# Optimization experiments

Measured on AMD Instinct MI355X. Metric: run time of the kernel, lower is better.

The kernel has to match this reference:

```python
import jax, jax.numpy as jnp
import numpy as np

B, A, F, C = 32, 64, 128, 128


def _mlp(h, W0, b0, W1, b1):
    # LinearLayer stack: Linear(2F->C) + ReLU, Linear(C->C) + ReLU
    h = jax.nn.relu(h @ W0 + b0)
    h = jax.nn.relu(h @ W1 + b1)
    return h


def setup_inputs() -> dict:
    key = jax.random.key(0)
    k0, k1, k2 = jax.random.split(key, 3)
    x = jax.random.normal(k0, (B, A, F), dtype=jnp.float32)
    W0 = jax.random.normal(k1, (2 * F, C), dtype=jnp.float32) * (1.0 / np.sqrt(2 * F))
    b0 = jnp.zeros((C,), dtype=jnp.float32)
    W1 = jax.random.normal(k2, (C, C), dtype=jnp.float32) * (1.0 / np.sqrt(C))
    b1 = jnp.zeros((C,), dtype=jnp.float32)
    return {"x": x, "W0": W0, "b0": b0, "W1": W1, "b1": b1}


def reference(x, W0, b0, W1, b1):
    nb, na, nf = x.shape
    # atom_tile[b,i,j]   = x[b,i]  (first atom of the pair)
    # atom_repeat[b,i,j] = x[b,j]  (second atom of the pair)
    xi = jnp.broadcast_to(x[:, :, None, :], (nb, na, na, nf))
    xj = jnp.broadcast_to(x[:, None, :, :], (nb, na, na, nf))
    # pair_x0 = cat(atom_tile, atom_repeat) = [x_i, x_j]
    p0 = jnp.concatenate([xi, xj], axis=-1).reshape(nb * na * na, 2 * nf)
    # pair_x1 = cat(atom_repeat, atom_tile) = [x_j, x_i]
    p1 = jnp.concatenate([xj, xi], axis=-1).reshape(nb * na * na, 2 * nf)
    h0 = _mlp(p0, W0, b0, W1, b1).reshape(nb, na * na, -1)
    h1 = _mlp(p1, W0, b0, W1, b1).reshape(nb, na * na, -1)
    return h0 + h1
```

## Files before the change

kernel.cpp:

```cpp
#include <hip/hip_runtime.h>
#include <hip/hip_bf16.h>

typedef float    f32x4 __attribute__((ext_vector_type(4)));
typedef _Float16 f16x4 __attribute__((ext_vector_type(4)));
typedef _Float16 f16x8 __attribute__((ext_vector_type(8)));
typedef unsigned int   u32x4 __attribute__((ext_vector_type(4)));

#define NB 32
#define NA 64
#define NF 128
#define NC 128

__global__ __launch_bounds__(256) void prep_kernel(
    const float* __restrict__ x, const float* __restrict__ W0,
    const float* __restrict__ b0, const float* __restrict__ W1,
    _Float16* __restrict__ u, _Float16* __restrict__ v,
    _Float16* __restrict__ w1f)
{
    int blk = blockIdx.x, tid = threadIdx.x;
    if (blk < 256) {
        __shared__ __align__(16) _Float16 w0h[32 * 64 * 8];
        int b = blk >> 3, g = (blk >> 1) & 3, half = blk & 1;

        int lane = tid & 63, wave = tid >> 6;
        int llo = lane & 15, lhi = lane >> 4;

        const float* xrow = x + ((size_t)b * NA + g * 16 + llo) * NF;
        f16x8 xf[4];
        #pragma unroll
        for (int kk = 0; kk < 4; ++kk) {
            f32x4 a0 = *(const f32x4*)(xrow + kk * 32 + lhi * 8);
            f32x4 a1 = *(const f32x4*)(xrow + kk * 32 + lhi * 8 + 4);
            #pragma unroll
            for (int e = 0; e < 4; ++e) {
                xf[kk][e]     = (_Float16)a0[e];
                xf[kk][e + 4] = (_Float16)a1[e];
            }
        }

        #pragma unroll
        for (int p = 0; p < 8; ++p) {
            int sl   = p * 256 + tid;
            int frag = sl >> 6;
            int ln   = sl & 63;
            int kk   = frag >> 3, nfc = frag & 7;
            int k0   = half * 128 + kk * 32 + (ln >> 4) * 8;
            int c    = nfc * 16 + (ln & 15);
            f16x8 o;
            #pragma unroll
            for (int e = 0; e < 8; ++e)
                o[e] = (_Float16)W0[(size_t)(k0 + e) * NC + c];
            *(f16x8*)(w0h + (size_t)sl * 8) = o;
        }
        __syncthreads();

        f32x4 acc[2];
        f32x4 z = {0.f, 0.f, 0.f, 0.f};
        acc[0] = z; acc[1] = z;
        #pragma unroll
        for (int kk = 0; kk < 4; ++kk) {
            #pragma unroll
            for (int t = 0; t < 2; ++t) {
                int nfc = wave * 2 + t;
                f16x8 aw = *(const f16x8*)(w0h +
                    (size_t)((kk * 8 + nfc) * 64 + lane) * 8);
                acc[t] = __builtin_amdgcn_mfma_f32_16x16x32_f16(
                    aw, xf[kk], acc[t], 0, 0, 0);
            }
        }

        _Float16* dst = half ? v : u;
        size_t arow = ((size_t)b * NA + g * 16 + llo) * NC;
        #pragma unroll
        for (int t = 0; t < 2; ++t) {
            int nfc = wave * 2 + t;
            int c0  = nfc * 16 + lhi * 4;
            f16x4 o;
            if (half) {
                f32x4 bb = *(const f32x4*)(b0 + c0);
                #pragma unroll
                for (int e = 0; e < 4; ++e)
                    o[e] = (_Float16)(acc[t][e] + bb[e]);
            } else {
                #pragma unroll
                for (int e = 0; e < 4; ++e)
                    o[e] = (_Float16)acc[t][e];
            }
            *(f16x4*)(dst + arow + c0) = o;
        }
    } else {
        int fl   = (blk - 256) * 256 + tid;
        int lane = fl & 63;
        int frag = fl >> 6;
        int kk = frag >> 3, nf = frag & 7;
        int k0 = kk * 32 + (lane >> 4) * 8;
        int n  = nf * 16 + (lane & 15);
        f16x8 o;
        #pragma unroll
        for (int e = 0; e < 8; ++e)
            o[e] = (_Float16)W1[(size_t)(k0 + e) * NC + n];
        *(f16x8*)(w1f + (size_t)fl * 8) = o;
    }
}

__global__ __launch_bounds__(256, 3) void pair_mlp_kernel(
    const float* __restrict__ b1g, const _Float16* __restrict__ u,
    const _Float16* __restrict__ v, const _Float16* __restrict__ w1f,
    float* __restrict__ out)
{
    __shared__ __align__(16) _Float16 u_s[16 * 128];
    __shared__ __align__(16) _Float16 v_s[16 * 128];
    __shared__ __align__(16) _Float16 w_s[32 * 64 * 8];

    int blk = blockIdx.x;
    int b = blk / 36;
    int t = blk % 36;
    int I = 0;
    while (t >= 8 - I) { t -= 8 - I; ++I; }
    int J = I + t;

    int tid = threadIdx.x;

    {
        int row = tid >> 4;
        int c   = tid & 15;
        int ga  = b * NA + ((row < 8) ? (I * 8 + row) : (J * 8 + (row & 7)));
        int sc  = row * 16 + (c ^ (row & 7));
        ((u32x4*)u_s)[sc] = ((const u32x4*)(u + (size_t)ga * NC))[c];
        ((u32x4*)v_s)[sc] = ((const u32x4*)(v + (size_t)ga * NC))[c];
    }
    #pragma unroll
    for (int p = 0; p < 8; ++p)
        ((u32x4*)w_s)[p * 256 + tid] = ((const u32x4*)w1f)[p * 256 + tid];
    __syncthreads();

    int wave = tid >> 6;
    int lane = tid & 63;
    int llo  = lane & 15;
    int lhi  = lane >> 4;
    int r    = wave * 16 + llo;
    int il   = r >> 3;
    int jl   = r & 7;

    f32x4 acc0[8], acc1[8];
    f32x4 z = {0.f, 0.f, 0.f, 0.f};
    #pragma unroll
    for (int nf = 0; nf < 8; ++nf) { acc0[nf] = z; acc1[nf] = z; }

    const f16x8* us = (const f16x8*)u_s;
    const f16x8* vs = (const f16x8*)v_s;
    const f16x8* wf = (const f16x8*)w_s;

    #pragma unroll
    for (int kk = 0; kk < 4; ++kk) {
        int kc  = kk * 4 + lhi;
        int scI = il * 16 + (kc ^ il);
        int scJ = (8 + jl) * 16 + (kc ^ jl);

        f16x8 uIv = us[scI];
        f16x8 vIv = vs[scI];
        f16x8 uJv = us[scJ];
        f16x8 vJv = vs[scJ];

        f16x8 s0 = uIv + vJv;
        f16x8 s1 = uJv + vIv;
        f16x8 h0, h1;
        #pragma unroll
        for (int e = 0; e < 8; ++e) {
            h0[e] = s0[e] < (_Float16)0 ? (_Float16)0 : s0[e];
            h1[e] = s1[e] < (_Float16)0 ? (_Float16)0 : s1[e];
        }

        #pragma unroll
        for (int nf = 0; nf < 8; ++nf) {
            f16x8 w = wf[(kk * 8 + nf) * 64 + lane];
            acc0[nf] = __builtin_amdgcn_mfma_f32_16x16x32_f16(w, h0, acc0[nf], 0, 0, 0);
            acc1[nf] = __builtin_amdgcn_mfma_f32_16x16x32_f16(w, h1, acc1[nf], 0, 0, 0);
        }
    }

    int Ig = I * 8 + il;
    int Jg = J * 8 + jl;
    float* p1 = out + ((size_t)b * 4096 + Ig * 64 + Jg) * 128 + lhi * 4;
    float* p2 = out + ((size_t)b * 4096 + Jg * 64 + Ig) * 128 + lhi * 4;
    bool mirror = (I != J);
    #pragma unroll
    for (int nf = 0; nf < 8; ++nf) {
        f32x4 bias = *(const f32x4*)(b1g + nf * 16 + lhi * 4);
        f32x4 val;
        #pragma unroll
        for (int e = 0; e < 4; ++e)
            val[e] = fmaxf(acc0[nf][e] + bias[e], 0.f) +
                     fmaxf(acc1[nf][e] + bias[e], 0.f);
        *(f32x4*)(p1 + nf * 16) = val;
        if (mirror)
            *(f32x4*)(p2 + nf * 16) = val;
    }
}

extern "C" void kernel_launch(void* const* d_in, const int* in_sizes, int n_in,
                              void* d_out, int out_size, void* d_ws, size_t ws_size,
                              hipStream_t stream)
{
    (void)in_sizes; (void)n_in; (void)out_size; (void)ws_size;
    const float* x  = (const float*)d_in[0];
    const float* W0 = (const float*)d_in[1];
    const float* b0 = (const float*)d_in[2];
    const float* W1 = (const float*)d_in[3];
    const float* b1 = (const float*)d_in[4];
    float* out = (float*)d_out;

    _Float16* u   = (_Float16*)d_ws;
    _Float16* v   = u + (size_t)NB * NA * NC;
    _Float16* w1f = v + (size_t)NB * NA * NC;

    prep_kernel<<<264, 256, 0, stream>>>(x, W0, b0, W1, u, v, w1f);
    pair_mlp_kernel<<<32 * 36, 256, 0, stream>>>(b1, u, v, w1f, out);
}
```

Before: 29.90 us.

## Keep W1 fragments in registers and drop symmetric-pair tiling in pair MLP

```diff
diff --git a/kernel.cpp b/kernel.cpp
--- a/kernel.cpp
+++ b/kernel.cpp
@@ -103,98 +103,93 @@
     }
 }
 
-__global__ __launch_bounds__(256, 3) void pair_mlp_kernel(
+__global__ __launch_bounds__(512, 2) void pair_mlp_kernel(
     const float* __restrict__ b1g, const _Float16* __restrict__ u,
     const _Float16* __restrict__ v, const _Float16* __restrict__ w1f,
     float* __restrict__ out)
 {
-    __shared__ __align__(16) _Float16 u_s[16 * 128];
-    __shared__ __align__(16) _Float16 v_s[16 * 128];
-    __shared__ __align__(16) _Float16 w_s[32 * 64 * 8];
+    __shared__ __align__(16) _Float16 u_s[64 * 128];
+    __shared__ __align__(16) _Float16 v_s[64 * 128];
 
     int blk = blockIdx.x;
-    int b = blk / 36;
-    int t = blk % 36;
-    int I = 0;
-    while (t >= 8 - I) { t -= 8 - I; ++I; }
-    int J = I + t;
-
-    int tid = threadIdx.x;
-
-    {
-        int row = tid >> 4;
-        int c   = tid & 15;
-        int ga  = b * NA + ((row < 8) ? (I * 8 + row) : (J * 8 + (row & 7)));
+    int b  = blk >> 3;
+    int Iq = blk & 7;
+    int tid  = threadIdx.x;
+    int wave = tid >> 6, lane = tid & 63;
+    int llo  = lane & 15, lhi = lane >> 4;
+
+    f16x8 wreg[4][8];
+    #pragma unroll
+    for (int kk = 0; kk < 4; ++kk)
+        #pragma unroll
+        for (int nf = 0; nf < 8; ++nf)
+            wreg[kk][nf] = ((const f16x8*)w1f)[(kk * 8 + nf) * 64 + lane];
+
+    #pragma unroll
+    for (int p = 0; p < 2; ++p) {
+        int idx = p * 512 + tid;
+        int row = idx >> 4;
+        int c   = idx & 15;
         int sc  = row * 16 + (c ^ (row & 7));
-        ((u32x4*)u_s)[sc] = ((const u32x4*)(u + (size_t)ga * NC))[c];
-        ((u32x4*)v_s)[sc] = ((const u32x4*)(v + (size_t)ga * NC))[c];
+        ((u32x4*)u_s)[sc] = ((const u32x4*)(u + ((size_t)b * NA + row) * NC))[c];
+        ((u32x4*)v_s)[sc] = ((const u32x4*)(v + ((size_t)b * NA + row) * NC))[c];
     }
-    #pragma unroll
-    for (int p = 0; p < 8; ++p)
-        ((u32x4*)w_s)[p * 256 + tid] = ((const u32x4*)w1f)[p * 256 + tid];
     __syncthreads();
 
-    int wave = tid >> 6;
-    int lane = tid & 63;
-    int llo  = lane & 15;
-    int lhi  = lane >> 4;
-    int r    = wave * 16 + llo;
-    int il   = r >> 3;
-    int jl   = r & 7;
-
-    f32x4 acc0[8], acc1[8];
-    f32x4 z = {0.f, 0.f, 0.f, 0.f};
-    #pragma unroll
-    for (int nf = 0; nf < 8; ++nf) { acc0[nf] = z; acc1[nf] = z; }
-
+    int ai = Iq * 8 + wave;
     const f16x8* us = (const f16x8*)u_s;
     const f16x8* vs = (const f16x8*)v_s;
-    const f16x8* wf = (const f16x8*)w_s;
-
-    #pragma unroll
-    for (int kk = 0; kk < 4; ++kk) {
-        int kc  = kk * 4 + lhi;
-        int scI = il * 16 + (kc ^ il);
-        int scJ = (8 + jl) * 16 + (kc ^ jl);
-
-        f16x8 uIv = us[scI];
-        f16x8 vIv = vs[scI];
-        f16x8 uJv = us[scJ];
-        f16x8 vJv = vs[scJ];
-
-        f16x8 s0 = uIv + vJv;
-        f16x8 s1 = uJv + vIv;
-        f16x8 h0, h1;
-        #pragma unroll
-        for (int e = 0; e < 8; ++e) {
-            h0[e] = s0[e] < (_Float16)0 ? (_Float16)0 : s0[e];
-            h1[e] = s1[e] < (_Float16)0 ? (_Float16)0 : s1[e];
-        }
-
+    float* orow = out + ((size_t)b * 4096 + (size_t)ai * 64) * 128;
+
+    f32x4 z = {0.f, 0.f, 0.f, 0.f};
+
+    for (int q = 0; q < 4; ++q) {
+        int aj = q * 16 + llo;
+
+        f32x4 acc0[8], acc1[8];
+        #pragma unroll
+        for (int nf = 0; nf < 8; ++nf) { acc0[nf] = z; acc1[nf] = z; }
+
+        #pragma unroll
+        for (int kk = 0; kk < 4; ++kk) {
+            int kc  = kk * 4 + lhi;
+            int sci = ai * 16 + (kc ^ (ai & 7));
+            int scj = aj * 16 + (kc ^ (aj & 7));
+
+            f16x8 ui = us[sci];
+            f16x8 vi = vs[sci];
+            f16x8 uj = us[scj];
+            f16x8 vj = vs[scj];
+
+            f16x8 s0 = ui + vj;
+            f16x8 s1 = uj + vi;
+            f16x8 h0, h1;
+            #pragma unroll
+            for (int e = 0; e < 8; ++e) {
+                h0[e] = s0[e] < (_Float16)0 ? (_Float16)0 : s0[e];
+                h1[e] = s1[e] < (_Float16)0 ? (_Float16)0 : s1[e];
+            }
+
+            #pragma unroll
+            for (int nf = 0; nf < 8; ++nf) {
+                acc0[nf] = __builtin_amdgcn_mfma_f32_16x16x32_f16(
+                    wreg[kk][nf], h0, acc0[nf], 0, 0, 0);
+                acc1[nf] = __builtin_amdgcn_mfma_f32_16x16x32_f16(
+                    wreg[kk][nf], h1, acc1[nf], 0, 0, 0);
+            }
+        }
+
+        float* p1 = orow + (size_t)(q * 16 + llo) * 128 + lhi * 4;
         #pragma unroll
         for (int nf = 0; nf < 8; ++nf) {
-            f16x8 w = wf[(kk * 8 + nf) * 64 + lane];
-            acc0[nf] = __builtin_amdgcn_mfma_f32_16x16x32_f16(w, h0, acc0[nf], 0, 0, 0);
-            acc1[nf] = __builtin_amdgcn_mfma_f32_16x16x32_f16(w, h1, acc1[nf], 0, 0, 0);
-        }
-    }
-
-    int Ig = I * 8 + il;
-    int Jg = J * 8 + jl;
-    float* p1 = out + ((size_t)b * 4096 + Ig * 64 + Jg) * 128 + lhi * 4;
-    float* p2 = out + ((size_t)b * 4096 + Jg * 64 + Ig) * 128 + lhi * 4;
-    bool mirror = (I != J);
-    #pragma unroll
-    for (int nf = 0; nf < 8; ++nf) {
-        f32x4 bias = *(const f32x4*)(b1g + nf * 16 + lhi * 4);
-        f32x4 val;
-        #pragma unroll
-        for (int e = 0; e < 4; ++e)
-            val[e] = fmaxf(acc0[nf][e] + bias[e], 0.f) +
-                     fmaxf(acc1[nf][e] + bias[e], 0.f);
-        *(f32x4*)(p1 + nf * 16) = val;
-        if (mirror)
-            *(f32x4*)(p2 + nf * 16) = val;
+            f32x4 bias = *(const f32x4*)(b1g + nf * 16 + lhi * 4);
+            f32x4 val;
+            #pragma unroll
+            for (int e = 0; e < 4; ++e)
+                val[e] = fmaxf(acc0[nf][e] + bias[e], 0.f) +
+                         fmaxf(acc1[nf][e] + bias[e], 0.f);
+            *(f32x4*)(p1 + nf * 16) = val;
+        }
     }
 }
 
@@ -215,5 +210,5 @@
     _Float16* w1f = v + (size_t)NB * NA * NC;
 
     prep_kernel<<<264, 256, 0, stream>>>(x, W0, b0, W1, u, v, w1f);
-    pair_mlp_kernel<<<32 * 36, 256, 0, stream>>>(b1, u, v, w1f, out);
+    pair_mlp_kernel<<<NB * 8, 512, 0, stream>>>(b1, u, v, w1f, out);
 }
```

Result: slower. 36.50 us (+22.1%).

## Fuse prep and pair-MLP kernels into one persistent kernel with grid barrier

Applied to the files above, without the earlier changes.

```diff
diff --git a/kernel.cpp b/kernel.cpp
--- a/kernel.cpp
+++ b/kernel.cpp
@@ -10,20 +10,28 @@
 #define NA 64
 #define NF 128
 #define NC 128
-
-__global__ __launch_bounds__(256) void prep_kernel(
+#define NBLK 576
+
+__global__ __launch_bounds__(256, 3) void fused_kernel(
     const float* __restrict__ x, const float* __restrict__ W0,
     const float* __restrict__ b0, const float* __restrict__ W1,
-    _Float16* __restrict__ u, _Float16* __restrict__ v,
-    _Float16* __restrict__ w1f)
+    const float* __restrict__ b1g, _Float16* __restrict__ u,
+    _Float16* __restrict__ v, _Float16* __restrict__ w1f,
+    unsigned int* __restrict__ cnt, float* __restrict__ out)
 {
+    __shared__ __align__(16) unsigned char smem[40960];
+    _Float16* w0h = (_Float16*)smem;
+    _Float16* u_s = (_Float16*)smem;
+    _Float16* v_s = (_Float16*)(smem + 4096);
+    _Float16* w_s = (_Float16*)(smem + 8192);
+
     int blk = blockIdx.x, tid = threadIdx.x;
+    int lane = tid & 63, wave = tid >> 6;
+    int llo = lane & 15, lhi = lane >> 4;
+    f32x4 z = {0.f, 0.f, 0.f, 0.f};
+
     if (blk < 256) {
-        __shared__ __align__(16) _Float16 w0h[32 * 64 * 8];
         int b = blk >> 3, g = (blk >> 1) & 3, half = blk & 1;
-
-        int lane = tid & 63, wave = tid >> 6;
-        int llo = lane & 15, lhi = lane >> 4;
 
         const float* xrow = x + ((size_t)b * NA + g * 16 + llo) * NF;
         f16x8 xf[4];
@@ -55,7 +63,6 @@
         __syncthreads();
 
         f32x4 acc[2];
-        f32x4 z = {0.f, 0.f, 0.f, 0.f};
         acc[0] = z; acc[1] = z;
         #pragma unroll
         for (int kk = 0; kk < 4; ++kk) {
@@ -88,113 +95,116 @@
             }
             *(f16x4*)(dst + arow + c0) = o;
         }
-    } else {
+    } else if (blk < 264) {
         int fl   = (blk - 256) * 256 + tid;
-        int lane = fl & 63;
+        int ln   = fl & 63;
         int frag = fl >> 6;
         int kk = frag >> 3, nf = frag & 7;
-        int k0 = kk * 32 + (lane >> 4) * 8;
-        int n  = nf * 16 + (lane & 15);
+        int k0 = kk * 32 + (ln >> 4) * 8;
+        int n  = nf * 16 + (ln & 15);
         f16x8 o;
         #pragma unroll
         for (int e = 0; e < 8; ++e)
             o[e] = (_Float16)W1[(size_t)(k0 + e) * NC + n];
         *(f16x8*)(w1f + (size_t)fl * 8) = o;
     }
-}
-
-__global__ __launch_bounds__(256, 3) void pair_mlp_kernel(
-    const float* __restrict__ b1g, const _Float16* __restrict__ u,
-    const _Float16* __restrict__ v, const _Float16* __restrict__ w1f,
-    float* __restrict__ out)
-{
-    __shared__ __align__(16) _Float16 u_s[16 * 128];
-    __shared__ __align__(16) _Float16 v_s[16 * 128];
-    __shared__ __align__(16) _Float16 w_s[32 * 64 * 8];
-
-    int blk = blockIdx.x;
-    int b = blk / 36;
-    int t = blk % 36;
-    int I = 0;
-    while (t >= 8 - I) { t -= 8 - I; ++I; }
-    int J = I + t;
-
-    int tid = threadIdx.x;
-
-    {
-        int row = tid >> 4;
-        int c   = tid & 15;
-        int ga  = b * NA + ((row < 8) ? (I * 8 + row) : (J * 8 + (row & 7)));
-        int sc  = row * 16 + (c ^ (row & 7));
-        ((u32x4*)u_s)[sc] = ((const u32x4*)(u + (size_t)ga * NC))[c];
-        ((u32x4*)v_s)[sc] = ((const u32x4*)(v + (size_t)ga * NC))[c];
+
+    __syncthreads();
+    if (tid == 0) {
+        __builtin_amdgcn_fence(__ATOMIC_RELEASE, "agent");
+        __hip_atomic_fetch_add(cnt, 1u, __ATOMIC_RELAXED,
+                               __HIP_MEMORY_SCOPE_AGENT);
+        while (__hip_atomic_load(cnt, __ATOMIC_RELAXED,
+                                 __HIP_MEMORY_SCOPE_AGENT) < NBLK)
+            __builtin_amdgcn_s_sleep(1);
+        __builtin_amdgcn_fence(__ATOMIC_ACQUIRE, "agent");
     }
+    __syncthreads();
+
     #pragma unroll
     for (int p = 0; p < 8; ++p)
         ((u32x4*)w_s)[p * 256 + tid] = ((const u32x4*)w1f)[p * 256 + tid];
-    __syncthreads();
-
-    int wave = tid >> 6;
-    int lane = tid & 63;
-    int llo  = lane & 15;
-    int lhi  = lane >> 4;
-    int r    = wave * 16 + llo;
-    int il   = r >> 3;
-    int jl   = r & 7;
-
-    f32x4 acc0[8], acc1[8];
-    f32x4 z = {0.f, 0.f, 0.f, 0.f};
-    #pragma unroll
-    for (int nf = 0; nf < 8; ++nf) { acc0[nf] = z; acc1[nf] = z; }
-
-    const f16x8* us = (const f16x8*)u_s;
-    const f16x8* vs = (const f16x8*)v_s;
-    const f16x8* wf = (const f16x8*)w_s;
-
-    #pragma unroll
-    for (int kk = 0; kk < 4; ++kk) {
-        int kc  = kk * 4 + lhi;
-        int scI = il * 16 + (kc ^ il);
-        int scJ = (8 + jl) * 16 + (kc ^ jl);
-
-        f16x8 uIv = us[scI];
-        f16x8 vIv = vs[scI];
-        f16x8 uJv = us[scJ];
-        f16x8 vJv = vs[scJ];
-
-        f16x8 s0 = uIv + vJv;
-        f16x8 s1 = uJv + vIv;
-        f16x8 h0, h1;
-        #pragma unroll
-        for (int e = 0; e < 8; ++e) {
-            h0[e] = s0[e] < (_Float16)0 ? (_Float16)0 : s0[e];
-            h1[e] = s1[e] < (_Float16)0 ? (_Float16)0 : s1[e];
-        }
-
+
+    #pragma unroll 1
+    for (int s = 0; s < 2; ++s) {
+        int task = blk * 2 + s;
+        int b = task / 36;
+        int t = task % 36;
+        int I = 0;
+        while (t >= 8 - I) { t -= 8 - I; ++I; }
+        int J = I + t;
+
+        if (s) __syncthreads();
+
+        {
+            int row = tid >> 4;
+            int c   = tid & 15;
+            int ga  = b * NA + ((row < 8) ? (I * 8 + row) : (J * 8 + (row & 7)));
+            int sc  = row * 16 + (c ^ (row & 7));
+            ((u32x4*)u_s)[sc] = ((const u32x4*)(u + (size_t)ga * NC))[c];
+            ((u32x4*)v_s)[sc] = ((const u32x4*)(v + (size_t)ga * NC))[c];
+        }
+        __syncthreads();
+
+        int r  = wave * 16 + llo;
+        int il = r >> 3;
+        int jl = r & 7;
+
+        f32x4 acc0[8], acc1[8];
+        #pragma unroll
+        for (int nf = 0; nf < 8; ++nf) { acc0[nf] = z; acc1[nf] = z; }
+
+        const f16x8* us = (const f16x8*)u_s;
+        const f16x8* vs = (const f16x8*)v_s;
+        const f16x8* wf = (const f16x8*)w_s;
+
+        #pragma unroll
+        for (int kk = 0; kk < 4; ++kk) {
+            int kc  = kk * 4 + lhi;
+            int scI = il * 16 + (kc ^ il);
+            int scJ = (8 + jl) * 16 + (kc ^ jl);
+
+            f16x8 uIv = us[scI];
+            f16x8 vIv = vs[scI];
+            f16x8 uJv = us[scJ];
+            f16x8 vJv = vs[scJ];
+
+            f16x8 s0 = uIv + vJv;
+            f16x8 s1 = uJv + vIv;
+            f16x8 h0, h1;
+            #pragma unroll
+            for (int e = 0; e < 8; ++e) {
+                h0[e] = s0[e] < (_Float16)0 ? (_Float16)0 : s0[e];
+                h1[e] = s1[e] < (_Float16)0 ? (_Float16)0 : s1[e];
+            }
+
+            #pragma unroll
+            for (int nf = 0; nf < 8; ++nf) {
+                f16x8 w = wf[(kk * 8 + nf) * 64 + lane];
+                acc0[nf] = __builtin_amdgcn_mfma_f32_16x16x32_f16(
+                    w, h0, acc0[nf], 0, 0, 0);
+                acc1[nf] = __builtin_amdgcn_mfma_f32_16x16x32_f16(
+                    w, h1, acc1[nf], 0, 0, 0);
+            }
+        }
+
+        int Ig = I * 8 + il;
+        int Jg = J * 8 + jl;
+        float* p1 = out + ((size_t)b * 4096 + Ig * 64 + Jg) * 128 + lhi * 4;
+        float* p2 = out + ((size_t)b * 4096 + Jg * 64 + Ig) * 128 + lhi * 4;
+        bool mirror = (I != J);
         #pragma unroll
         for (int nf = 0; nf < 8; ++nf) {
-            f16x8 w = wf[(kk * 8 + nf) * 64 + lane];
-            acc0[nf] = __builtin_amdgcn_mfma_f32_16x16x32_f16(w, h0, acc0[nf], 0, 0, 0);
-            acc1[nf] = __builtin_amdgcn_mfma_f32_16x16x32_f16(w, h1, acc1[nf], 0, 0, 0);
-        }
-    }
-
-    int Ig = I * 8 + il;
-    int Jg = J * 8 + jl;
-    float* p1 = out + ((size_t)b * 4096 + Ig * 64 + Jg) * 128 + lhi * 4;
-    float* p2 = out + ((size_t)b * 4096 + Jg * 64 + Ig) * 128 + lhi * 4;
-    bool mirror = (I != J);
-    #pragma unroll
-    for (int nf = 0; nf < 8; ++nf) {
-        f32x4 bias = *(const f32x4*)(b1g + nf * 16 + lhi * 4);
-        f32x4 val;
-        #pragma unroll
-        for (int e = 0; e < 4; ++e)
-            val[e] = fmaxf(acc0[nf][e] + bias[e], 0.f) +
-                     fmaxf(acc1[nf][e] + bias[e], 0.f);
-        *(f32x4*)(p1 + nf * 16) = val;
-        if (mirror)
-            *(f32x4*)(p2 + nf * 16) = val;
+            f32x4 bias = *(const f32x4*)(b1g + nf * 16 + lhi * 4);
+            f32x4 val;
+            #pragma unroll
+            for (int e = 0; e < 4; ++e)
+                val[e] = fmaxf(acc0[nf][e] + bias[e], 0.f) +
+                         fmaxf(acc1[nf][e] + bias[e], 0.f);
+            *(f32x4*)(p1 + nf * 16) = val;
+            if (mirror)
+                *(f32x4*)(p2 + nf * 16) = val;
+        }
     }
 }
 
@@ -213,7 +223,9 @@
     _Float16* u   = (_Float16*)d_ws;
     _Float16* v   = u + (size_t)NB * NA * NC;
     _Float16* w1f = v + (size_t)NB * NA * NC;
-
-    prep_kernel<<<264, 256, 0, stream>>>(x, W0, b0, W1, u, v, w1f);
-    pair_mlp_kernel<<<32 * 36, 256, 0, stream>>>(b1, u, v, w1f, out);
+    unsigned int* cnt = (unsigned int*)(w1f + 32 * 64 * 8);
+
+    hipMemsetAsync(cnt, 0, sizeof(unsigned int), stream);
+    fused_kernel<<<NBLK, 256, 0, stream>>>(x, W0, b0, W1, b1, u, v, w1f,
+                                           cnt, out);
 }
```

After: 79.76 us. 167% more time.

## Process two pair tiles per block and coalesce W0 staging via swizzled LDS

Applied to the files above, without the earlier changes.

```diff
diff --git a/kernel.cpp b/kernel.cpp
--- a/kernel.cpp
+++ b/kernel.cpp
@@ -18,12 +18,12 @@
     _Float16* __restrict__ w1f)
 {
     int blk = blockIdx.x, tid = threadIdx.x;
+    int lane = tid & 63, wave = tid >> 6;
+    int llo = lane & 15, lhi = lane >> 4;
+
     if (blk < 256) {
-        __shared__ __align__(16) _Float16 w0h[32 * 64 * 8];
+        __shared__ __align__(16) _Float16 w0l[128 * 128];
         int b = blk >> 3, g = (blk >> 1) & 3, half = blk & 1;
-
-        int lane = tid & 63, wave = tid >> 6;
-        int llo = lane & 15, lhi = lane >> 4;
 
         const float* xrow = x + ((size_t)b * NA + g * 16 + llo) * NF;
         f16x8 xf[4];
@@ -38,19 +38,22 @@
             }
         }
 
+        const float* w0src = W0 + (size_t)half * 128 * NC;
         #pragma unroll
         for (int p = 0; p < 8; ++p) {
-            int sl   = p * 256 + tid;
-            int frag = sl >> 6;
-            int ln   = sl & 63;
-            int kk   = frag >> 3, nfc = frag & 7;
-            int k0   = half * 128 + kk * 32 + (ln >> 4) * 8;
-            int c    = nfc * 16 + (ln & 15);
+            int idx = p * 256 + tid;
+            int k   = idx >> 4;
+            int ch  = idx & 15;
+            f32x4 a0 = *(const f32x4*)(w0src + (size_t)k * NC + ch * 8);
+            f32x4 a1 = *(const f32x4*)(w0src + (size_t)k * NC + ch * 8 + 4);
             f16x8 o;
             #pragma unroll
-            for (int e = 0; e < 8; ++e)
-                o[e] = (_Float16)W0[(size_t)(k0 + e) * NC + c];
-            *(f16x8*)(w0h + (size_t)sl * 8) = o;
+            for (int e = 0; e < 4; ++e) {
+                o[e]     = (_Float16)a0[e];
+                o[e + 4] = (_Float16)a1[e];
+            }
+            int sc = (ch ^ ((k >> 3) & 7)) << 3;
+            *(f16x8*)(w0l + k * 128 + sc) = o;
         }
         __syncthreads();
 
@@ -62,8 +65,16 @@
             #pragma unroll
             for (int t = 0; t < 2; ++t) {
                 int nfc = wave * 2 + t;
-                f16x8 aw = *(const f16x8*)(w0h +
-                    (size_t)((kk * 8 + nfc) * 64 + lane) * 8);
+                int c   = nfc * 16 + llo;
+                int chx = (c >> 3);
+                int cl  = c & 7;
+                f16x8 aw;
+                #pragma unroll
+                for (int e = 0; e < 8; ++e) {
+                    int k = kk * 32 + lhi * 8 + e;
+                    int sc = ((chx ^ ((k >> 3) & 7)) << 3) | cl;
+                    aw[e] = w0l[k * 128 + sc];
+                }
                 acc[t] = __builtin_amdgcn_mfma_f32_16x16x32_f16(
                     aw, xf[kk], acc[t], 0, 0, 0);
             }
@@ -90,11 +101,11 @@
         }
     } else {
         int fl   = (blk - 256) * 256 + tid;
-        int lane = fl & 63;
+        int ln   = fl & 63;
         int frag = fl >> 6;
         int kk = frag >> 3, nf = frag & 7;
-        int k0 = kk * 32 + (lane >> 4) * 8;
-        int n  = nf * 16 + (lane & 15);
+        int k0 = kk * 32 + (ln >> 4) * 8;
+        int n  = nf * 16 + (ln & 15);
         f16x8 o;
         #pragma unroll
         for (int e = 0; e < 8; ++e)
@@ -103,7 +114,7 @@
     }
 }
 
-__global__ __launch_bounds__(256, 3) void pair_mlp_kernel(
+__global__ __launch_bounds__(256, 4) void pair_mlp_kernel(
     const float* __restrict__ b1g, const _Float16* __restrict__ u,
     const _Float16* __restrict__ v, const _Float16* __restrict__ w1f,
     float* __restrict__ out)
@@ -112,89 +123,95 @@
     __shared__ __align__(16) _Float16 v_s[16 * 128];
     __shared__ __align__(16) _Float16 w_s[32 * 64 * 8];
 
-    int blk = blockIdx.x;
-    int b = blk / 36;
-    int t = blk % 36;
-    int I = 0;
-    while (t >= 8 - I) { t -= 8 - I; ++I; }
-    int J = I + t;
-
-    int tid = threadIdx.x;
-
-    {
-        int row = tid >> 4;
-        int c   = tid & 15;
-        int ga  = b * NA + ((row < 8) ? (I * 8 + row) : (J * 8 + (row & 7)));
-        int sc  = row * 16 + (c ^ (row & 7));
-        ((u32x4*)u_s)[sc] = ((const u32x4*)(u + (size_t)ga * NC))[c];
-        ((u32x4*)v_s)[sc] = ((const u32x4*)(v + (size_t)ga * NC))[c];
-    }
+    int blk = blockIdx.x, tid = threadIdx.x;
+    int wave = tid >> 6, lane = tid & 63;
+    int llo  = lane & 15, lhi = lane >> 4;
+    f32x4 z = {0.f, 0.f, 0.f, 0.f};
+
     #pragma unroll
     for (int p = 0; p < 8; ++p)
         ((u32x4*)w_s)[p * 256 + tid] = ((const u32x4*)w1f)[p * 256 + tid];
-    __syncthreads();
-
-    int wave = tid >> 6;
-    int lane = tid & 63;
-    int llo  = lane & 15;
-    int lhi  = lane >> 4;
-    int r    = wave * 16 + llo;
-    int il   = r >> 3;
-    int jl   = r & 7;
-
-    f32x4 acc0[8], acc1[8];
-    f32x4 z = {0.f, 0.f, 0.f, 0.f};
-    #pragma unroll
-    for (int nf = 0; nf < 8; ++nf) { acc0[nf] = z; acc1[nf] = z; }
-
-    const f16x8* us = (const f16x8*)u_s;
-    const f16x8* vs = (const f16x8*)v_s;
-    const f16x8* wf = (const f16x8*)w_s;
-
-    #pragma unroll
-    for (int kk = 0; kk < 4; ++kk) {
-        int kc  = kk * 4 + lhi;
-        int scI = il * 16 + (kc ^ il);
-        int scJ = (8 + jl) * 16 + (kc ^ jl);
-
-        f16x8 uIv = us[scI];
-        f16x8 vIv = vs[scI];
-        f16x8 uJv = us[scJ];
-        f16x8 vJv = vs[scJ];
-
-        f16x8 s0 = uIv + vJv;
-        f16x8 s1 = uJv + vIv;
-        f16x8 h0, h1;
-        #pragma unroll
-        for (int e = 0; e < 8; ++e) {
-            h0[e] = s0[e] < (_Float16)0 ? (_Float16)0 : s0[e];
-            h1[e] = s1[e] < (_Float16)0 ? (_Float16)0 : s1[e];
-        }
-
+
+    #pragma unroll 1
+    for (int s = 0; s < 2; ++s) {
+        int task = blk * 2 + s;
+        int b = task / 36;
+        int t = task % 36;
+        int I = 0;
+        while (t >= 8 - I) { t -= 8 - I; ++I; }
+        int J = I + t;
+
+        if (s) __syncthreads();
+
+        {
+            int row = tid >> 4;
+            int c   = tid & 15;
+            int ga  = b * NA + ((row < 8) ? (I * 8 + row) : (J * 8 + (row & 7)));
+            int sc  = row * 16 + (c ^ (row & 7));
+            ((u32x4*)u_s)[sc] = ((const u32x4*)(u + (size_t)ga * NC))[c];
+            ((u32x4*)v_s)[sc] = ((const u32x4*)(v + (size_t)ga * NC))[c];
+        }
+        __syncthreads();
+
+        int r  = wave * 16 + llo;
+        int il = r >> 3;
+        int jl = r & 7;
+
+        f32x4 acc0[8], acc1[8];
+        #pragma unroll
+        for (int nf = 0; nf < 8; ++nf) { acc0[nf] = z; acc1[nf] = z; }
+
+        const f16x8* us = (const f16x8*)u_s;
+        const f16x8* vs = (const f16x8*)v_s;
+        const f16x8* wf = (const f16x8*)w_s;
+
+        #pragma unroll
+        for (int kk = 0; kk < 4; ++kk) {
+            int kc  = kk * 4 + lhi;
+            int scI = il * 16 + (kc ^ il);
+            int scJ = (8 + jl) * 16 + (kc ^ jl);
+
+            f16x8 uIv = us[scI];
+            f16x8 vIv = vs[scI];
+            f16x8 uJv = us[scJ];
+            f16x8 vJv = vs[scJ];
+
+            f16x8 s0 = uIv + vJv;
+            f16x8 s1 = uJv + vIv;
+            f16x8 h0, h1;
+            #pragma unroll
+            for (int e = 0; e < 8; ++e) {
+                h0[e] = s0[e] < (_Float16)0 ? (_Float16)0 : s0[e];
+                h1[e] = s1[e] < (_Float16)0 ? (_Float16)0 : s1[e];
+            }
+
+            #pragma unroll
+            for (int nf = 0; nf < 8; ++nf) {
+                f16x8 w = wf[(kk * 8 + nf) * 64 + lane];
+                acc0[nf] = __builtin_amdgcn_mfma_f32_16x16x32_f16(
+                    w, h0, acc0[nf], 0, 0, 0);
+                acc1[nf] = __builtin_amdgcn_mfma_f32_16x16x32_f16(
+                    w, h1, acc1[nf], 0, 0, 0);
+            }
+        }
+
+        int Ig = I * 8 + il;
+        int Jg = J * 8 + jl;
+        float* p1 = out + ((size_t)b * 4096 + Ig * 64 + Jg) * 128 + lhi * 4;
+        float* p2 = out + ((size_t)b * 4096 + Jg * 64 + Ig) * 128 + lhi * 4;
+        bool mirror = (I != J);
         #pragma unroll
         for (int nf = 0; nf < 8; ++nf) {
-            f16x8 w = wf[(kk * 8 + nf) * 64 + lane];
-            acc0[nf] = __builtin_amdgcn_mfma_f32_16x16x32_f16(w, h0, acc0[nf], 0, 0, 0);
-            acc1[nf] = __builtin_amdgcn_mfma_f32_16x16x32_f16(w, h1, acc1[nf], 0, 0, 0);
-        }
-    }
-
-    int Ig = I * 8 + il;
-    int Jg = J * 8 + jl;
-    float* p1 = out + ((size_t)b * 4096 + Ig * 64 + Jg) * 128 + lhi * 4;
-    float* p2 = out + ((size_t)b * 4096 + Jg * 64 + Ig) * 128 + lhi * 4;
-    bool mirror = (I != J);
-    #pragma unroll
-    for (int nf = 0; nf < 8; ++nf) {
-        f32x4 bias = *(const f32x4*)(b1g + nf * 16 + lhi * 4);
-        f32x4 val;
-        #pragma unroll
-        for (int e = 0; e < 4; ++e)
-            val[e] = fmaxf(acc0[nf][e] + bias[e], 0.f) +
-                     fmaxf(acc1[nf][e] + bias[e], 0.f);
-        *(f32x4*)(p1 + nf * 16) = val;
-        if (mirror)
-            *(f32x4*)(p2 + nf * 16) = val;
+            f32x4 bias = *(const f32x4*)(b1g + nf * 16 + lhi * 4);
+            f32x4 val;
+            #pragma unroll
+            for (int e = 0; e < 4; ++e)
+                val[e] = fmaxf(acc0[nf][e] + bias[e], 0.f) +
+                         fmaxf(acc1[nf][e] + bias[e], 0.f);
+            *(f32x4*)(p1 + nf * 16) = val;
+            if (mirror)
+                *(f32x4*)(p2 + nf * 16) = val;
+        }
     }
 }
 
@@ -215,5 +232,5 @@
     _Float16* w1f = v + (size_t)NB * NA * NC;
 
     prep_kernel<<<264, 256, 0, stream>>>(x, W0, b0, W1, u, v, w1f);
-    pair_mlp_kernel<<<32 * 36, 256, 0, stream>>>(b1, u, v, w1f, out);
+    pair_mlp_kernel<<<576, 256, 0, stream>>>(b1, u, v, w1f, out);
 }
```

New measurement: 40.25 us. 1.35x slower.
